# Optimization experiments

Measured on AMD Instinct MI355X. Metric: run time of the kernel, lower is better.

## Reference

```python
import jax, jax.numpy as jnp
import numpy as np

EPS = 1e-6


def setup_inputs() -> dict:
    key = jax.random.key(0)
    ks = jax.random.split(key, 6)
    B, T, C, H, D, M = 1, 2048, 1024, 16, 64, 64
    return {
        "x": jax.random.normal(ks[0], (B, T, C), dtype=jnp.float32),
        "w_qkv": jax.random.normal(ks[1], (C, 3 * C), dtype=jnp.float32) * (1.0 / np.sqrt(C)),
        "b_qkv": jax.random.normal(ks[2], (3 * C,), dtype=jnp.float32) * 0.02,
        "w_out": jax.random.normal(ks[3], (C, C), dtype=jnp.float32) * (1.0 / np.sqrt(C)),
        "b_out": jax.random.normal(ks[4], (C,), dtype=jnp.float32) * 0.02,
        "proj": jax.random.normal(ks[5], (H, D, M), dtype=jnp.float32),
    }


def _feature_map(x, proj):
    # x: [B,H,T,D], proj: [H,D,M] -> [B,H,T,M]
    M = proj.shape[-1]
    p = jnp.einsum("bhtd,hdm->bhtm", x, proj)
    return jax.nn.relu(p) / jnp.sqrt(jnp.float32(M))


def reference(x, w_qkv, b_qkv, w_out, b_out, proj):
    B, T, C = x.shape
    H, D, M = proj.shape
    qkv = x @ w_qkv + b_qkv                        # [B,T,3C]
    q, k, v = jnp.split(qkv, 3, axis=-1)
    # [B,T,C] -> [B,H,T,D]
    to_heads = lambda t: t.reshape(B, T, H, D).transpose(0, 2, 1, 3)
    q, k, v = to_heads(q), to_heads(k), to_heads(v)

    q_prime = _feature_map(q, proj)                # [B,H,T,M]
    k_prime = _feature_map(k, proj)                # [B,H,T,M]

    # causal linear attention: cumulative sum of outer products k' v^T
    kv_prod = jnp.einsum("bhtm,bhtd->bhtmd", k_prime, v)   # [B,H,T,M,D]
    kv_cumsum = jnp.cumsum(kv_prod, axis=2)
    context = jnp.einsum("bhtm,bhtmd->bhtd", q_prime, kv_cumsum)

    k_cumsum = jnp.cumsum(k_prime, axis=2)                   # [B,H,T,M]
    norm = jnp.einsum("bhtm,bhtm->bht", q_prime, k_cumsum)
    out = context / (norm[..., None] + EPS)                  # [B,H,T,D]

    out = out.transpose(0, 2, 1, 3).reshape(B, T, C)
    return out @ w_out + b_out
```

## Files before the change

kernel.cpp:

```cpp
#include <hip/hip_runtime.h>
#include <hip/hip_bf16.h>

#define TT 2048
#define CC 1024
#define HH 16
#define DD 64
#define FM 64
#define NCH 32
#define CL 64
#define N_QKV 3072
#define EPSV 1e-6f

#define OFF_KVT 0u
#define OFF_KS  2097152u
#define OFF_Z   2129920u
#define OFF_U16 2162688u
#define U_QBF 0u
#define U_KBF 2097152u
#define U_VT  4194304u
#define U_QP  6291456u
#define U_KP  8388608u
#define U_ST  12582912u
#define U_XBF 14680064u
#define U_WQT 16777216u
#define U_WOT 19922944u

typedef __attribute__((ext_vector_type(8))) short bf16x8;
typedef __attribute__((ext_vector_type(4))) float f32x4;
typedef __attribute__((ext_vector_type(4))) unsigned short u16x4;

__device__ __forceinline__ unsigned short f2bf(float f) {
  unsigned int u = __float_as_uint(f);
  u = (u + 0x7fffu + ((u >> 16) & 1u)) >> 16;
  return (unsigned short)u;
}
__device__ __forceinline__ float bf2f(unsigned short b) {
  return __uint_as_float(((unsigned)b) << 16);
}

__device__ __forceinline__ void gload16(const void* g, void* l) {
  __builtin_amdgcn_global_load_lds(
      (const __attribute__((address_space(1))) unsigned int*)g,
      (__attribute__((address_space(3))) unsigned int*)l, 16, 0, 0);
}

__device__ __forceinline__ void stage_tile64(const unsigned short* g, unsigned rowstride,
                                             unsigned short* lds, int w, int lane) {
  const int l8 = lane >> 3, l7 = lane & 7;
  const int kcg = (l7 ^ l8) * 8;
#pragma unroll
  for (int jj = 0; jj < 2; ++jj) {
    const int inst = w * 2 + jj;
    const int row = inst * 8 + l8;
    gload16(&g[(unsigned)row * rowstride + kcg], &lds[inst * 512]);
  }
}

__device__ __forceinline__ bf16x8 frag64(const unsigned short* lds, int r, int kchunk) {
  const int slot = kchunk ^ (r & 7);
  return *reinterpret_cast<const bf16x8*>(&lds[r * 64 + slot * 8]);
}

__device__ __forceinline__ void transpose64_dev(const float* __restrict__ src,
                                                unsigned short* __restrict__ dst,
                                                int K, int N, int k0, int n0,
                                                float (*T)[68], int tid) {
#pragma unroll
  for (int it = 0; it < 4; ++it) {
    int f = tid + it * 256;
    int r = f >> 4, c4 = (f & 15) * 4;
    float4 v = *reinterpret_cast<const float4*>(&src[(unsigned)(k0 + r) * N + n0 + c4]);
    T[r][c4 + 0] = v.x; T[r][c4 + 1] = v.y;
    T[r][c4 + 2] = v.z; T[r][c4 + 3] = v.w;
  }
  __syncthreads();
#pragma unroll
  for (int it = 0; it < 4; ++it) {
    int f = tid + it * 256;
    int nl = f >> 4, kq = (f & 15) * 4;
    u16x4 o;
#pragma unroll
    for (int j = 0; j < 4; ++j) o[j] = f2bf(T[kq + j][nl]);
    *reinterpret_cast<u16x4*>(&dst[(unsigned)(n0 + nl) * K + k0 + kq]) = o;
  }
}

__global__ __launch_bounds__(256) void k_prep(const float* __restrict__ x,
                                              const float* __restrict__ wq,
                                              const float* __restrict__ wo,
                                              unsigned short* __restrict__ xbf,
                                              unsigned short* __restrict__ wqT,
                                              unsigned short* __restrict__ woT) {
  __shared__ float T[64][68];
  const int tid = threadIdx.x;
  int b = blockIdx.x;
  if (b < 2048) {
    unsigned i = (unsigned)b * 1024u + (unsigned)tid * 4u;
    float4 v = *reinterpret_cast<const float4*>(&x[i]);
    u16x4 o;
    o[0] = f2bf(v.x); o[1] = f2bf(v.y); o[2] = f2bf(v.z); o[3] = f2bf(v.w);
    *reinterpret_cast<u16x4*>(&xbf[i]) = o;
    return;
  }
  b -= 2048;
  if (b < 768) {
    transpose64_dev(wq, wqT, CC, N_QKV, (b / 48) * 64, (b % 48) * 64, T, tid);
    return;
  }
  b -= 768;
  transpose64_dev(wo, woT, CC, CC, (b / 16) * 64, (b % 16) * 64, T, tid);
}

__global__ __launch_bounds__(256) void k_qkv_mfma(const unsigned short* __restrict__ Xbf,
                                                  const unsigned short* __restrict__ WqT,
                                                  const float* __restrict__ bias,
                                                  unsigned short* __restrict__ qbf,
                                                  unsigned short* __restrict__ kbf,
                                                  unsigned short* __restrict__ vt) {
  __shared__ unsigned short As[64 * 64];
  __shared__ unsigned short Bs[128 * 64];
  const int tid = threadIdx.x, lane = tid & 63, w = tid >> 6;
  const int wm = w >> 1, wn = w & 1;
  int lin = blockIdx.y * 24 + blockIdx.x;
  int swz = (lin & 7) * 96 + (lin >> 3);
  const int bx = swz % 24, by = swz / 24;
  const int m0b = by * 64, n0b = bx * 128;
  const int l8 = lane >> 3, l7 = lane & 7;
  const int kcg = (l7 ^ l8) * 8;
  f32x4 acc[2][4] = {};
  for (int k0 = 0; k0 < CC; k0 += 64) {
    if (k0) __syncthreads();
#pragma unroll
    for (int jj = 0; jj < 2; ++jj) {
      const int inst = w * 2 + jj;
      const int row = inst * 8 + l8;
      gload16(&Xbf[(unsigned)(m0b + row) * CC + k0 + kcg], &As[inst * 512]);
    }
#pragma unroll
    for (int jj = 0; jj < 4; ++jj) {
      const int inst = w * 4 + jj;
      const int row = inst * 8 + l8;
      gload16(&WqT[(unsigned)(n0b + row) * CC + k0 + kcg], &Bs[inst * 512]);
    }
    __syncthreads();
#pragma unroll
    for (int kk = 0; kk < 2; ++kk) {
      bf16x8 af[2], bg[4];
#pragma unroll
      for (int i = 0; i < 2; ++i) {
        const int r = wm * 32 + i * 16 + (lane & 15);
        const int slot = (kk * 4 + (lane >> 4)) ^ (r & 7);
        af[i] = *reinterpret_cast<const bf16x8*>(&As[r * 64 + slot * 8]);
      }
#pragma unroll
      for (int j = 0; j < 4; ++j) {
        const int r = wn * 64 + j * 16 + (lane & 15);
        const int slot = (kk * 4 + (lane >> 4)) ^ (r & 7);
        bg[j] = *reinterpret_cast<const bf16x8*>(&Bs[r * 64 + slot * 8]);
      }
#pragma unroll
      for (int i = 0; i < 2; ++i)
#pragma unroll
        for (int j = 0; j < 4; ++j)
          acc[i][j] = __builtin_amdgcn_mfma_f32_16x16x32_bf16(af[i], bg[j],
                                                              acc[i][j], 0, 0, 0);
    }
  }
  const int m0 = m0b + wm * 32;
  const int n0w = n0b + wn * 64;
  const int sel = n0w >> 10;
  const int h = (n0w & 1023) >> 6;
#pragma unroll
  for (int i = 0; i < 2; ++i) {
    const int t0 = m0 + i * 16 + (lane >> 4) * 4;
#pragma unroll
    for (int j = 0; j < 4; ++j) {
      const int n = n0w + j * 16 + (lane & 15);
      const float bv = bias[n];
      const int d = n & 63;
      if (sel == 2) {
        u16x4 o;
#pragma unroll
        for (int r = 0; r < 4; ++r) o[r] = f2bf(acc[i][j][r] + bv);
        *reinterpret_cast<u16x4*>(&vt[((unsigned)h * 64 + d) * TT + t0]) = o;
      } else {
        unsigned short* dst = (sel ? kbf : qbf) + (unsigned)h * TT * 64 + d;
#pragma unroll
        for (int r = 0; r < 4; ++r)
          dst[(unsigned)(t0 + r) * 64] = f2bf(acc[i][j][r] + bv);
      }
    }
  }
}

__global__ __launch_bounds__(256) void k_feat(const float* __restrict__ proj,
                                              const unsigned short* __restrict__ qbf,
                                              const unsigned short* __restrict__ kbf,
                                              const unsigned short* __restrict__ vt,
                                              unsigned short* __restrict__ qp,
                                              unsigned short* __restrict__ kp,
                                              float* __restrict__ kvt,
                                              float* __restrict__ ksum) {
  __shared__ unsigned short Xs[4096];
  __shared__ float Pj[4096];
  __shared__ unsigned short Os[4096];
  __shared__ unsigned short VTs[4096];
  const int tid = threadIdx.x, lane = tid & 63, w = tid >> 6;
  const int c = blockIdx.x, h = blockIdx.y, which = blockIdx.z;
  const unsigned short* src = (which ? kbf : qbf) + ((unsigned)h * TT + c * 64) * 64;
  stage_tile64(src, 64, Xs, w, lane);
  if (which) stage_tile64(vt + (unsigned)h * 64 * TT + (unsigned)c * 64, TT, VTs, w, lane);
#pragma unroll
  for (int it = 0; it < 4; ++it) {
    const unsigned idx = (unsigned)(tid + it * 256) * 4u;
    *reinterpret_cast<f32x4*>(&Pj[idx]) =
        *reinterpret_cast<const f32x4*>(&proj[(unsigned)h * 4096 + idx]);
  }
  __syncthreads();
  const int mrow = w * 16 + (lane & 15);
  bf16x8 af[2];
#pragma unroll
  for (int kk = 0; kk < 2; ++kk)
#pragma unroll
    for (int e = 0; e < 8; ++e) {
      const int d = (lane >> 4) * 8 + kk * 32 + e;
      af[kk][e] = (short)f2bf(Pj[d * 64 + mrow]);
    }
  f32x4 accf[4] = {};
#pragma unroll
  for (int j = 0; j < 4; ++j)
#pragma unroll
    for (int kk = 0; kk < 2; ++kk)
      accf[j] = __builtin_amdgcn_mfma_f32_16x16x32_bf16(
          af[kk], frag64(Xs, j * 16 + (lane & 15), kk * 4 + (lane >> 4)), accf[j], 0, 0, 0);
#pragma unroll
  for (int j = 0; j < 4; ++j)
#pragma unroll
    for (int r = 0; r < 4; ++r) {
      float v = accf[j][r];
      accf[j][r] = (v > 0.f ? v : 0.f) * 0.125f;
    }
#pragma unroll
  for (int j = 0; j < 4; ++j) {
    const int t = j * 16 + (lane & 15);
#pragma unroll
    for (int r = 0; r < 4; ++r) {
      const int m = w * 16 + (lane >> 4) * 4 + r;
      Os[t * 64 + (((m >> 3) ^ (t & 7)) * 8) + (m & 7)] = f2bf(accf[j][r]);
    }
  }
  if (which) {
    float rs[4];
#pragma unroll
    for (int r = 0; r < 4; ++r) {
      float s = accf[0][r] + accf[1][r] + accf[2][r] + accf[3][r];
#pragma unroll
      for (int off = 1; off < 16; off <<= 1) s += __shfl_xor(s, off, 64);
      rs[r] = s;
    }
    if ((lane & 15) == 0) {
#pragma unroll
      for (int r = 0; r < 4; ++r) {
        const int m = w * 16 + (lane >> 4) * 4 + r;
        ksum[((unsigned)h * NCH + c) * 64u + m] = rs[r];
      }
    }
  }
  __syncthreads();
  unsigned short* dst = (which ? kp : qp) + ((unsigned)h * TT + c * 64) * 64;
  {
    const int t = tid >> 2;
#pragma unroll
    for (int q = 0; q < 2; ++q) {
      const int chunk = (tid & 3) * 2 + q;
      bf16x8 vle = *reinterpret_cast<const bf16x8*>(&Os[t * 64 + ((chunk ^ (t & 7)) * 8)]);
      *reinterpret_cast<bf16x8*>(&dst[t * 64 + chunk * 8]) = vle;
    }
  }
  if (which) {
    const int m = w * 16 + (lane & 15);
    bf16x8 afm[2];
#pragma unroll
    for (int kk = 0; kk < 2; ++kk)
#pragma unroll
      for (int e = 0; e < 8; ++e) {
        const int t = kk * 32 + (lane >> 4) * 8 + e;
        afm[kk][e] = (short)Os[t * 64 + (((m >> 3) ^ (t & 7)) << 3) + (m & 7)];
      }
    f32x4 acckv[4] = {};
#pragma unroll
    for (int j = 0; j < 4; ++j)
#pragma unroll
      for (int kk = 0; kk < 2; ++kk)
        acckv[j] = __builtin_amdgcn_mfma_f32_16x16x32_bf16(
            afm[kk], frag64(VTs, j * 16 + (lane & 15), kk * 4 + (lane >> 4)), acckv[j], 0, 0, 0);
    float* dkv = kvt + ((unsigned)h * NCH + c) * 4096u;
#pragma unroll
    for (int j = 0; j < 4; ++j) {
      const int d = j * 16 + (lane & 15);
      const int mq = w * 16 + (lane >> 4) * 4;
      *reinterpret_cast<f32x4*>(&dkv[(unsigned)d * 64 + mq]) = acckv[j];
    }
  }
}

__global__ __launch_bounds__(256) void k_prefix(const float* __restrict__ kvt,
                                                const float* __restrict__ ksum,
                                                unsigned short* __restrict__ st,
                                                float* __restrict__ z) {
  const int h = blockIdx.y;
  const unsigned e = blockIdx.x * 256u + threadIdx.x;
  float run = 0.f;
#pragma unroll
  for (int c = 0; c < NCH; ++c) {
    const unsigned idx = ((unsigned)h * NCH + c) * 4096u + e;
    st[idx] = f2bf(run);
    run += kvt[idx];
  }
  if (blockIdx.x == 0 && threadIdx.x < 64) {
    float zr = 0.f;
#pragma unroll
    for (int c = 0; c < NCH; ++c) {
      const unsigned idx = ((unsigned)h * NCH + c) * 64u + threadIdx.x;
      z[idx] = zr;
      zr += ksum[idx];
    }
  }
}

__global__ __launch_bounds__(256) void k_attn(const unsigned short* __restrict__ qp,
                                              const unsigned short* __restrict__ kp,
                                              const unsigned short* __restrict__ vt,
                                              const unsigned short* __restrict__ st,
                                              const float* __restrict__ z,
                                              unsigned short* __restrict__ attnb) {
  __shared__ unsigned short QPs[4096];
  __shared__ unsigned short KPs[4096];
  __shared__ unsigned short VTs[4096];
  __shared__ unsigned short STs[4096];
  __shared__ float zsm[64];
  __shared__ float nsm[64];
  const int tid = threadIdx.x, lane = tid & 63, w = tid >> 6;
  const int c = blockIdx.x, h = blockIdx.y;
  stage_tile64(qp + ((unsigned)h * TT + c * 64) * 64, 64, QPs, w, lane);
  stage_tile64(kp + ((unsigned)h * TT + c * 64) * 64, 64, KPs, w, lane);
  stage_tile64(vt + (unsigned)h * 64 * TT + (unsigned)c * 64, TT, VTs, w, lane);
  stage_tile64(st + ((unsigned)h * NCH + c) * 4096u, 64, STs, w, lane);
  if (tid < 64) zsm[tid] = z[((unsigned)h * NCH + c) * 64u + tid];
  __syncthreads();
  const int tr = w * 16 + (lane & 15);
  bf16x8 afq[2];
#pragma unroll
  for (int kk = 0; kk < 2; ++kk) afq[kk] = frag64(QPs, tr, kk * 4 + (lane >> 4));
  f32x4 accA[4] = {};
#pragma unroll
  for (int j = 0; j < 4; ++j)
#pragma unroll
    for (int kk = 0; kk < 2; ++kk)
      accA[j] = __builtin_amdgcn_mfma_f32_16x16x32_bf16(
          afq[kk], frag64(KPs, j * 16 + (lane & 15), kk * 4 + (lane >> 4)), accA[j], 0, 0, 0);
  float rs[4] = {0.f, 0.f, 0.f, 0.f};
#pragma unroll
  for (int j = 0; j < 4; ++j) {
    const int s = j * 16 + (lane & 15);
#pragma unroll
    for (int r = 0; r < 4; ++r) {
      const int t = w * 16 + (lane >> 4) * 4 + r;
      float v = (s <= t) ? accA[j][r] : 0.f;
      accA[j][r] = v;
      rs[r] += v;
    }
  }
#pragma unroll
  for (int r = 0; r < 4; ++r)
#pragma unroll
    for (int off = 1; off < 16; off <<= 1) rs[r] += __shfl_xor(rs[r], off, 64);
  __syncthreads();
  if ((lane & 15) == 0) {
#pragma unroll
    for (int r = 0; r < 4; ++r) nsm[w * 16 + (lane >> 4) * 4 + r] = rs[r];
  }
#pragma unroll
  for (int j = 0; j < 4; ++j) {
    const int s = j * 16 + (lane & 15);
#pragma unroll
    for (int r = 0; r < 4; ++r) {
      const int t = w * 16 + (lane >> 4) * 4 + r;
      KPs[t * 64 + (((s >> 3) ^ (t & 7)) * 8) + (s & 7)] = f2bf(accA[j][r]);
    }
  }
  __syncthreads();
  {
    const int t = tid >> 2, part = tid & 3;
    float qz = 0.f;
#pragma unroll
    for (int mm = 0; mm < 16; ++mm) {
      const int m = part * 16 + mm;
      qz += bf2f(QPs[t * 64 + (((m >> 3) ^ (t & 7)) * 8) + (m & 7)]) * zsm[m];
    }
    qz += __shfl_xor(qz, 1, 64);
    qz += __shfl_xor(qz, 2, 64);
    if (part == 0) nsm[t] += qz + EPSV;
  }
  bf16x8 afa[2];
#pragma unroll
  for (int kk = 0; kk < 2; ++kk) afa[kk] = frag64(KPs, tr, kk * 4 + (lane >> 4));
  f32x4 acc[4] = {};
#pragma unroll
  for (int j = 0; j < 4; ++j) {
    const int br = j * 16 + (lane & 15);
#pragma unroll
    for (int kk = 0; kk < 2; ++kk) {
      acc[j] = __builtin_amdgcn_mfma_f32_16x16x32_bf16(
          afa[kk], frag64(VTs, br, kk * 4 + (lane >> 4)), acc[j], 0, 0, 0);
      acc[j] = __builtin_amdgcn_mfma_f32_16x16x32_bf16(
          afq[kk], frag64(STs, br, kk * 4 + (lane >> 4)), acc[j], 0, 0, 0);
    }
  }
  __syncthreads();
#pragma unroll
  for (int j = 0; j < 4; ++j) {
    const int d = j * 16 + (lane & 15);
#pragma unroll
    for (int r = 0; r < 4; ++r) {
      const int t = w * 16 + (lane >> 4) * 4 + r;
      attnb[(unsigned)(c * 64 + t) * CC + h * 64 + d] = f2bf(acc[j][r] / nsm[t]);
    }
  }
}

__global__ __launch_bounds__(256) void k_out_mfma(const unsigned short* __restrict__ Abf,
                                                  const unsigned short* __restrict__ WoT,
                                                  const float* __restrict__ bias,
                                                  float* __restrict__ out) {
  __shared__ unsigned short As[4096];
  __shared__ unsigned short Bs[4096];
  const int tid = threadIdx.x, lane = tid & 63, w = tid >> 6;
  const int wm = w >> 1, wn = w & 1;
  int lin = blockIdx.y * 16 + blockIdx.x;
  int swz = (lin & 7) * 64 + (lin >> 3);
  const int bx = swz & 15, by = swz >> 4;
  const int m0 = by * 64, n0 = bx * 64;
  const int l8 = lane >> 3, l7 = lane & 7;
  const int kcg = (l7 ^ l8) * 8;
  f32x4 acc[2][2] = {};
  for (int k0 = 0; k0 < CC; k0 += 64) {
    if (k0) __syncthreads();
#pragma unroll
    for (int jj = 0; jj < 2; ++jj) {
      const int inst = w * 2 + jj;
      const int row = inst * 8 + l8;
      gload16(&Abf[(unsigned)(m0 + row) * CC + k0 + kcg], &As[inst * 512]);
      gload16(&WoT[(unsigned)(n0 + row) * CC + k0 + kcg], &Bs[inst * 512]);
    }
    __syncthreads();
#pragma unroll
    for (int kk = 0; kk < 2; ++kk) {
      bf16x8 af[2], bg[2];
#pragma unroll
      for (int i = 0; i < 2; ++i) {
        const int r = wm * 32 + i * 16 + (lane & 15);
        const int slot = (kk * 4 + (lane >> 4)) ^ (r & 7);
        af[i] = *reinterpret_cast<const bf16x8*>(&As[r * 64 + slot * 8]);
      }
#pragma unroll
      for (int j = 0; j < 2; ++j) {
        const int r = wn * 32 + j * 16 + (lane & 15);
        const int slot = (kk * 4 + (lane >> 4)) ^ (r & 7);
        bg[j] = *reinterpret_cast<const bf16x8*>(&Bs[r * 64 + slot * 8]);
      }
#pragma unroll
      for (int i = 0; i < 2; ++i)
#pragma unroll
        for (int j = 0; j < 2; ++j)
          acc[i][j] = __builtin_amdgcn_mfma_f32_16x16x32_bf16(af[i], bg[j],
                                                              acc[i][j], 0, 0, 0);
    }
  }
#pragma unroll
  for (int i = 0; i < 2; ++i) {
#pragma unroll
    for (int j = 0; j < 2; ++j) {
      const int n = n0 + wn * 32 + j * 16 + (lane & 15);
      const float bv = bias[n];
#pragma unroll
      for (int r = 0; r < 4; ++r) {
        const int m = m0 + wm * 32 + i * 16 + (lane >> 4) * 4 + r;
        out[(unsigned)m * CC + n] = acc[i][j][r] + bv;
      }
    }
  }
}

extern "C" void kernel_launch(void* const* d_in, const int* in_sizes, int n_in,
                              void* d_out, int out_size, void* d_ws, size_t ws_size,
                              hipStream_t stream) {
  const float* x = (const float*)d_in[0];
  const float* w_qkv = (const float*)d_in[1];
  const float* b_qkv = (const float*)d_in[2];
  const float* w_out = (const float*)d_in[3];
  const float* b_out = (const float*)d_in[4];
  const float* proj = (const float*)d_in[5];
  float* ws = (float*)d_ws;
  float* out = (float*)d_out;
  float* kvt = ws + OFF_KVT;
  float* ksum = ws + OFF_KS;
  float* zf = ws + OFF_Z;
  unsigned short* ub = (unsigned short*)(ws + OFF_U16);
  unsigned short* qbf = ub + U_QBF;
  unsigned short* kbf = ub + U_KBF;
  unsigned short* vt = ub + U_VT;
  unsigned short* qp = ub + U_QP;
  unsigned short* kp = ub + U_KP;
  unsigned short* st = ub + U_ST;
  unsigned short* xbf = ub + U_XBF;
  unsigned short* wqT = ub + U_WQT;
  unsigned short* woT = ub + U_WOT;
  unsigned short* attnb = xbf;
  dim3 blk(256, 1, 1);
  k_prep<<<dim3(3072), blk, 0, stream>>>(x, w_qkv, w_out, xbf, wqT, woT);
  k_qkv_mfma<<<dim3(N_QKV / 128, TT / 64), blk, 0, stream>>>(xbf, wqT, b_qkv, qbf, kbf, vt);
  k_feat<<<dim3(NCH, HH, 2), blk, 0, stream>>>(proj, qbf, kbf, vt, qp, kp, kvt, ksum);
  k_prefix<<<dim3(16, HH), blk, 0, stream>>>(kvt, ksum, st, zf);
  k_attn<<<dim3(NCH, HH), blk, 0, stream>>>(qp, kp, vt, st, zf, attnb);
  k_out_mfma<<<dim3(CC / 64, TT / 64), blk, 0, stream>>>(attnb, woT, b_out, out);
}
```

Measured before the change: 71.93 us.

## Stage QKV epilogue through LDS for coalesced stores; store per-chunk KV in bf16

The QKV GEMM epilogue now writes each wave's bias-added bf16 tile into a swizzled LDS buffer that reuses the GEMM's shared memory. It then emits 16-byte coalesced stores for q/k rows and for the transposed v layout, replacing the strided 2-byte scalar stores. Separately, the per-chunk KV outer-product sums are written as bf16 instead of fp32, halving that intermediate's traffic in k_feat and k_prefix. The workspace layout is reshuffled to match. The bf16 KV partials lose precision before the fp32 prefix accumulation, and the LDS staging adds an extra barrier.

```diff
diff --git a/kernel.cpp b/kernel.cpp
--- a/kernel.cpp
+++ b/kernel.cpp
@@ -11,15 +11,15 @@
 #define N_QKV 3072
 #define EPSV 1e-6f
 
-#define OFF_KVT 0u
-#define OFF_KS  2097152u
-#define OFF_Z   2129920u
-#define OFF_U16 2162688u
-#define U_QBF 0u
-#define U_KBF 2097152u
-#define U_VT  4194304u
-#define U_QP  6291456u
-#define U_KP  8388608u
+#define OFF_KS  0u
+#define OFF_Z   32768u
+#define OFF_U16 65536u
+#define U_KVT 0u
+#define U_QBF 2097152u
+#define U_KBF 4194304u
+#define U_VT  6291456u
+#define U_QP  8388608u
+#define U_KP  10485760u
 #define U_ST  12582912u
 #define U_XBF 14680064u
 #define U_WQT 16777216u
@@ -117,8 +117,9 @@
                                                   unsigned short* __restrict__ qbf,
                                                   unsigned short* __restrict__ kbf,
                                                   unsigned short* __restrict__ vt) {
-  __shared__ unsigned short As[64 * 64];
-  __shared__ unsigned short Bs[128 * 64];
+  __shared__ unsigned short LDSU[12288];
+  unsigned short* As = LDSU;
+  unsigned short* Bs = LDSU + 4096;
   const int tid = threadIdx.x, lane = tid & 63, w = tid >> 6;
   const int wm = w >> 1, wn = w & 1;
   int lin = blockIdx.y * 24 + blockIdx.x;
@@ -166,29 +167,47 @@
                                                               acc[i][j], 0, 0, 0);
     }
   }
-  const int m0 = m0b + wm * 32;
   const int n0w = n0b + wn * 64;
   const int sel = n0w >> 10;
   const int h = (n0w & 1023) >> 6;
-#pragma unroll
-  for (int i = 0; i < 2; ++i) {
-    const int t0 = m0 + i * 16 + (lane >> 4) * 4;
+  const int t0w = m0b + wm * 32;
+  float bvj[4];
+#pragma unroll
+  for (int j = 0; j < 4; ++j) bvj[j] = bias[n0w + j * 16 + (lane & 15)];
+  __syncthreads();
+  unsigned short* myT = LDSU + w * 2048;
+#pragma unroll
+  for (int i = 0; i < 2; ++i)
 #pragma unroll
     for (int j = 0; j < 4; ++j) {
-      const int n = n0w + j * 16 + (lane & 15);
-      const float bv = bias[n];
-      const int d = n & 63;
-      if (sel == 2) {
-        u16x4 o;
-#pragma unroll
-        for (int r = 0; r < 4; ++r) o[r] = f2bf(acc[i][j][r] + bv);
-        *reinterpret_cast<u16x4*>(&vt[((unsigned)h * 64 + d) * TT + t0]) = o;
-      } else {
-        unsigned short* dst = (sel ? kbf : qbf) + (unsigned)h * TT * 64 + d;
-#pragma unroll
-        for (int r = 0; r < 4; ++r)
-          dst[(unsigned)(t0 + r) * 64] = f2bf(acc[i][j][r] + bv);
-      }
+      const int d = j * 16 + (lane & 15);
+#pragma unroll
+      for (int r = 0; r < 4; ++r) {
+        const int t = i * 16 + (lane >> 4) * 4 + r;
+        myT[t * 64 + (((d >> 3) ^ (t & 7)) << 3) + (d & 7)] = f2bf(acc[i][j][r] + bvj[j]);
+      }
+    }
+  if (sel == 2) {
+#pragma unroll
+    for (int q = 0; q < 4; ++q) {
+      const int cid = q * 64 + lane;
+      const int d = cid >> 2, tc = cid & 3;
+      bf16x8 o;
+#pragma unroll
+      for (int e = 0; e < 8; ++e) {
+        const int t = tc * 8 + e;
+        o[e] = (short)myT[t * 64 + (((d >> 3) ^ (t & 7)) << 3) + (d & 7)];
+      }
+      *reinterpret_cast<bf16x8*>(&vt[((unsigned)h * 64 + d) * TT + t0w + tc * 8]) = o;
+    }
+  } else {
+    unsigned short* dst0 = (sel ? kbf : qbf) + ((unsigned)h * TT + (unsigned)t0w) * 64u;
+#pragma unroll
+    for (int q = 0; q < 4; ++q) {
+      const int cid = q * 64 + lane;
+      const int t = cid >> 3, dc = cid & 7;
+      bf16x8 o = *reinterpret_cast<const bf16x8*>(&myT[t * 64 + ((dc ^ (t & 7)) << 3)]);
+      *reinterpret_cast<bf16x8*>(&dst0[(unsigned)cid * 8]) = o;
     }
   }
 }
@@ -199,7 +218,7 @@
                                               const unsigned short* __restrict__ vt,
                                               unsigned short* __restrict__ qp,
                                               unsigned short* __restrict__ kp,
-                                              float* __restrict__ kvt,
+                                              unsigned short* __restrict__ kvt,
                                               float* __restrict__ ksum) {
   __shared__ unsigned short Xs[4096];
   __shared__ float Pj[4096];
@@ -294,17 +313,20 @@
       for (int kk = 0; kk < 2; ++kk)
         acckv[j] = __builtin_amdgcn_mfma_f32_16x16x32_bf16(
             afm[kk], frag64(VTs, j * 16 + (lane & 15), kk * 4 + (lane >> 4)), acckv[j], 0, 0, 0);
-    float* dkv = kvt + ((unsigned)h * NCH + c) * 4096u;
+    unsigned short* dkv = kvt + ((unsigned)h * NCH + c) * 4096u;
 #pragma unroll
     for (int j = 0; j < 4; ++j) {
       const int d = j * 16 + (lane & 15);
       const int mq = w * 16 + (lane >> 4) * 4;
-      *reinterpret_cast<f32x4*>(&dkv[(unsigned)d * 64 + mq]) = acckv[j];
-    }
-  }
-}
-
-__global__ __launch_bounds__(256) void k_prefix(const float* __restrict__ kvt,
+      u16x4 o;
+#pragma unroll
+      for (int r = 0; r < 4; ++r) o[r] = f2bf(acckv[j][r]);
+      *reinterpret_cast<u16x4*>(&dkv[(unsigned)d * 64 + mq]) = o;
+    }
+  }
+}
+
+__global__ __launch_bounds__(256) void k_prefix(const unsigned short* __restrict__ kvt,
                                                 const float* __restrict__ ksum,
                                                 unsigned short* __restrict__ st,
                                                 float* __restrict__ z) {
@@ -315,7 +337,7 @@
   for (int c = 0; c < NCH; ++c) {
     const unsigned idx = ((unsigned)h * NCH + c) * 4096u + e;
     st[idx] = f2bf(run);
-    run += kvt[idx];
+    run += bf2f(kvt[idx]);
   }
   if (blockIdx.x == 0 && threadIdx.x < 64) {
     float zr = 0.f;
@@ -503,10 +525,10 @@
   const float* proj = (const float*)d_in[5];
   float* ws = (float*)d_ws;
   float* out = (float*)d_out;
-  float* kvt = ws + OFF_KVT;
   float* ksum = ws + OFF_KS;
   float* zf = ws + OFF_Z;
   unsigned short* ub = (unsigned short*)(ws + OFF_U16);
+  unsigned short* kvt = ub + U_KVT;
   unsigned short* qbf = ub + U_QBF;
   unsigned short* kbf = ub + U_KBF;
   unsigned short* vt = ub + U_VT;
```

Result: no change. 70.53 us (-1.9%).
